# Optimization experiments

Hardware: AMD Instinct MI355X
Metric: run time of the kernel (lower is better)

Reference implementation:

```python
import jax, jax.numpy as jnp
import numpy as np

EMBED_DIM = 1024
NUM_HEADS = 16
HEAD_DIM = EMBED_DIM // NUM_HEADS
LN_EPS = 1e-5


def setup_inputs() -> dict:
    key = jax.random.key(0)
    ks = jax.random.split(key, 5)
    N, L, C = 32, 577, EMBED_DIM
    x = jax.random.normal(ks[0], (N, L, C), dtype=jnp.float32)
    ln1_g = jnp.ones((C,), dtype=jnp.float32)
    ln1_b = jnp.zeros((C,), dtype=jnp.float32)
    w_in = jax.random.normal(ks[1], (3 * C, C), dtype=jnp.float32) * (C ** -0.5)
    b_in = jax.random.normal(ks[2], (3 * C,), dtype=jnp.float32) * 0.02
    w_out = jax.random.normal(ks[3], (C, C), dtype=jnp.float32) * (C ** -0.5)
    b_out = jax.random.normal(ks[4], (C,), dtype=jnp.float32) * 0.02
    return {"x": x, "ln1_g": ln1_g, "ln1_b": ln1_b, "w_in": w_in,
            "b_in": b_in, "w_out": w_out, "b_out": b_out}


def _layernorm(x, g, b):
    mu = jnp.mean(x, axis=-1, keepdims=True)
    var = jnp.mean(jnp.square(x - mu), axis=-1, keepdims=True)
    return (x - mu) * jax.lax.rsqrt(var + LN_EPS) * g + b


def reference(x, ln1_g, ln1_b, w_in, b_in, w_out, b_out):
    # ClearCLIP last block, attn_variant='qq', keep_residual=False, keep_ffn=False.
    N, L, C = x.shape
    H, D = NUM_HEADS, HEAD_DIM
    z = _layernorm(x, ln1_g, ln1_b)
    qkv = z @ w_in.T + b_in                      # (N, L, 3C)
    q, k, v = jnp.split(qkv, 3, axis=-1)
    k = q                                        # 'qq' self-self variant
    def heads(t):
        return t.reshape(N, L, H, D).transpose(0, 2, 1, 3)  # (N, H, L, D)
    q, k, v = heads(q), heads(k), heads(v)
    scale = 1.0 / np.sqrt(D).astype(np.float32)
    scores = jnp.einsum('nhld,nhsd->nhls', q, k) * scale    # (N, H, L, L)
    attn = jax.nn.softmax(scores, axis=-1)
    out = jnp.einsum('nhls,nhsd->nhld', attn, v)            # (N, H, L, D)
    out = out.transpose(0, 2, 1, 3).reshape(N, L, C)
    return out @ w_out.T + b_out                 # ls_1 = Identity, no residual/FFN
```

## Files before the change

### kernel.cpp

```cpp
#include <hip/hip_runtime.h>
#include <stdint.h>

typedef short bf16x8 __attribute__((ext_vector_type(8)));
typedef float f32x4 __attribute__((ext_vector_type(4)));
typedef unsigned int uint4v __attribute__((ext_vector_type(4)));
typedef unsigned short ushort4v __attribute__((ext_vector_type(4)));
typedef float float4v __attribute__((ext_vector_type(4)));

#define MROWS 18464
#define SEQ   577
#define CDIM  1024
#define SPAD  640
#define W1ELEMS (2048*1024)
#define W2ELEMS (1024*1024)
#define SQC 0.42466089f

__device__ __forceinline__ unsigned short f2bf(float f) {
  unsigned int u = __float_as_uint(f);
  u += 0x7fffu + ((u >> 16) & 1u);
  return (unsigned short)(u >> 16);
}

__device__ __forceinline__ void load_lds16(const void* g, void* lds) {
  __builtin_amdgcn_global_load_lds(
      (const __attribute__((address_space(1))) unsigned int*)(uint64_t)(uintptr_t)g,
      (__attribute__((address_space(3))) unsigned int*)(unsigned int)(uintptr_t)lds,
      16, 0, 0);
}

__global__ __launch_bounds__(256) void ln_kernel(const float* __restrict__ x,
                                                 const float* __restrict__ g,
                                                 const float* __restrict__ b,
                                                 unsigned short* __restrict__ z) {
  const int row = blockIdx.x;
  const int t = threadIdx.x;
  const float4v v = *(const float4v*)(x + (size_t)row * CDIM + t * 4);
  float s  = v[0] + v[1] + v[2] + v[3];
  float ss = v[0]*v[0] + v[1]*v[1] + v[2]*v[2] + v[3]*v[3];
  #pragma unroll
  for (int off = 1; off < 64; off <<= 1) { s += __shfl_xor(s, off); ss += __shfl_xor(ss, off); }
  __shared__ float rs[4], rss[4];
  const int w = t >> 6, l = t & 63;
  if (l == 0) { rs[w] = s; rss[w] = ss; }
  __syncthreads();
  s = rs[0] + rs[1] + rs[2] + rs[3];
  ss = rss[0] + rss[1] + rss[2] + rss[3];
  const float mu = s * (1.0f / CDIM);
  const float var = ss * (1.0f / CDIM) - mu * mu;
  const float rstd = rsqrtf(var + 1e-5f);
  const float4v gv = *(const float4v*)(g + t * 4);
  const float4v bv = *(const float4v*)(b + t * 4);
  ushort4v o;
  #pragma unroll
  for (int j = 0; j < 4; ++j) o[j] = f2bf((v[j] - mu) * rstd * gv[j] + bv[j]);
  *(ushort4v*)(z + (size_t)row * CDIM + t * 4) = o;
}

__global__ __launch_bounds__(256) void conv_kernel(const float* __restrict__ w_in,
                                                   const float* __restrict__ w_out,
                                                   unsigned short* __restrict__ wqv,
                                                   unsigned short* __restrict__ wo,
                                                   unsigned short* __restrict__ vt) {
  const int idx = blockIdx.x * 256 + threadIdx.x;
  const int e = idx * 4;
  if (e < W1ELEMS) {
    const int row = e >> 10;
    const int srow = row < 1024 ? row : row + 1024;
    const float4v v = *(const float4v*)(w_in + (size_t)srow * 1024 + (e & 1023));
    ushort4v o;
    #pragma unroll
    for (int j = 0; j < 4; ++j) o[j] = f2bf(v[j]);
    *(ushort4v*)(wqv + e) = o;
  } else if (e < W1ELEMS + W2ELEMS) {
    const int e2 = e - W1ELEMS;
    const float4v v = *(const float4v*)(w_out + e2);
    ushort4v o;
    #pragma unroll
    for (int j = 0; j < 4; ++j) o[j] = f2bf(v[j]);
    *(ushort4v*)(wo + e2) = o;
  } else {
    const int pidx = idx - (W1ELEMS + W2ELEMS) / 4;
    const int ic = pidx >> 3, part = pidx & 7;
    *(uint4v*)(vt + (size_t)ic * SPAD + 576 + part * 8) = (uint4v)0u;
  }
}

template<int MODE>
__global__ __launch_bounds__(512, 2) void gemm256(const unsigned short* __restrict__ A,
                                                  const unsigned short* __restrict__ B,
                                                  const float* __restrict__ bias,
                                                  void* __restrict__ outp,
                                                  unsigned short* __restrict__ vtout) {
  __shared__ char smem[131072];
  const int t = threadIdx.x;
  const int w = t >> 6, l = t & 63;
  int p, c;
  if constexpr (MODE == 0) {
    const int L = (blockIdx.x & 7) * 73 + (blockIdx.x >> 3);
    p = L >> 3; c = L & 7;
  } else {
    const int xcd = blockIdx.x & 7, j = blockIdx.x >> 3;
    const int L = (xcd < 4 ? xcd * 37 : 148 + (xcd - 4) * 36) + j;
    p = L >> 2; c = L & 3;
  }
  const int m0 = p * 256;
  const int n0 = c * 256;
  const int wm = w >> 2, wn = w & 3;
  const int g4 = (l >> 4) * 4;
  const int fr = l & 15;
  const int fb = (l >> 4) * 16;
  const int sw = (l & 7) << 4;

  f32x4 acc[8][4];
  #pragma unroll
  for (int i = 0; i < 8; ++i)
    #pragma unroll
    for (int j = 0; j < 4; ++j) acc[i][j] = (f32x4)0.0f;

  const int srow = l >> 3;
  const int scol = ((((l & 7) * 16) ^ ((srow & 7) << 4)) >> 1);
  const unsigned short* Ap[4];
  const unsigned short* Bp[4];
  #pragma unroll
  for (int c2 = 0; c2 < 4; ++c2) {
    int arow = m0 + w * 32 + c2 * 8 + srow;
    if (arow > MROWS - 1) arow = MROWS - 1;
    Ap[c2] = A + (size_t)arow * 1024 + scol;
    Bp[c2] = B + (size_t)(n0 + w * 32 + c2 * 8 + srow) * 1024 + scol;
  }

  #define STG(kt, buf)                                                     \
    {                                                                      \
      char* const d_ = smem + (buf) * 65536 + w * 4096;                    \
      const int k0_ = (kt) * 64;                                           \
      _Pragma("unroll")                                                    \
      for (int c2 = 0; c2 < 4; ++c2) {                                     \
        load_lds16(Ap[c2] + k0_, d_ + c2 * 1024);                          \
        load_lds16(Bp[c2] + k0_, d_ + 32768 + c2 * 1024);                  \
      }                                                                    \
    }

  STG(0, 0)
  __syncthreads();

  for (int kb = 0; kb < 16; ++kb) {
    const int b = kb & 1;
    if (kb < 15) STG(kb + 1, b ^ 1)
    const char* Ab = smem + b * 65536;
    const char* Bb = Ab + 32768;
    #pragma unroll
    for (int kk = 0; kk < 2; ++kk) {
      bf16x8 af[8], bfr[4];
      #pragma unroll
      for (int i = 0; i < 8; ++i)
        af[i] = *(const bf16x8*)(Ab + (wm * 128 + i * 16 + fr) * 128 + ((kk * 64 + fb) ^ sw));
      #pragma unroll
      for (int j = 0; j < 4; ++j)
        bfr[j] = *(const bf16x8*)(Bb + (wn * 64 + j * 16 + fr) * 128 + ((kk * 64 + fb) ^ sw));
      #pragma unroll
      for (int i = 0; i < 8; ++i)
        #pragma unroll
        for (int j = 0; j < 4; ++j)
          acc[i][j] = __builtin_amdgcn_mfma_f32_16x16x32_bf16(af[i], bfr[j], acc[i][j], 0, 0, 0);
    }
    __syncthreads();
  }
  #undef STG

  if constexpr (MODE == 0) {
    unsigned short* sm = (unsigned short*)smem;
    const bool isq = (n0 < 1024);
    const float* bb = isq ? (bias + n0) : (bias + 1024 + n0);
    const float scl = isq ? SQC : 1.0f;
    float bcol[4];
    #pragma unroll
    for (int j = 0; j < 4; ++j) bcol[j] = bb[wn * 64 + j * 16 + fr];
    for (int pass = 0; pass < 2; ++pass) {
      if (wm == pass) {
        #pragma unroll
        for (int i = 0; i < 8; ++i)
          #pragma unroll
          for (int j = 0; j < 4; ++j)
            #pragma unroll
            for (int r = 0; r < 4; ++r)
              sm[(i * 16 + g4 + r) * 264 + wn * 64 + j * 16 + fr] =
                  f2bf((acc[i][j][r] + bcol[j]) * scl);
      }
      __syncthreads();
      if (isq) {
        unsigned short* o = (unsigned short*)outp;
        #pragma unroll
        for (int it = 0; it < 8; ++it) {
          const int cid = it * 512 + t;
          const int row = cid >> 5, ch = cid & 31;
          const int grow = m0 + pass * 128 + row;
          if (grow < MROWS)
            *(uint4v*)(o + (size_t)grow * 1024 + n0 + ch * 8) =
                *(const uint4v*)(sm + row * 264 + ch * 8);
        }
      } else {
        const int rowloc = t & 127, chb = t >> 7;
        const int token = m0 + pass * 128 + rowloc;
        if (token < MROWS) {
          const unsigned int nimg = (unsigned int)token / 577u;
          const int s = token - (int)(nimg * 577u);
          unsigned short* op =
              vtout + ((size_t)nimg * 1024 + (n0 - 1024) + chb * 64) * SPAD + s;
          const unsigned short* sp = sm + rowloc * 264 + chb * 64;
          #pragma unroll 8
          for (int it = 0; it < 64; ++it)
            op[(size_t)it * SPAD] = sp[it];
        }
      }
      __syncthreads();
    }
  } else {
    float* smf = (float*)smem;
    float bcol[4];
    #pragma unroll
    for (int j = 0; j < 4; ++j) bcol[j] = bias[n0 + wn * 64 + j * 16 + fr];
    float* o = (float*)outp;
    for (int q4 = 0; q4 < 4; ++q4) {
      if (wm == (q4 >> 1)) {
        const int i0 = (q4 & 1) * 4;
        #pragma unroll
        for (int i2 = 0; i2 < 4; ++i2)
          #pragma unroll
          for (int j = 0; j < 4; ++j)
            #pragma unroll
            for (int r = 0; r < 4; ++r)
              smf[(i2 * 16 + g4 + r) * 260 + wn * 64 + j * 16 + fr] =
                  acc[i0 + i2][j][r] + bcol[j];
      }
      __syncthreads();
      #pragma unroll
      for (int it = 0; it < 8; ++it) {
        const int cid = it * 512 + t;
        const int row = cid >> 6, ch = cid & 63;
        const int grow = m0 + q4 * 64 + row;
        if (grow < MROWS)
          *(float4v*)(o + (size_t)grow * 1024 + n0 + ch * 4) =
              *(const float4v*)(smf + row * 260 + ch * 4);
      }
      __syncthreads();
    }
  }
}

__global__ __launch_bounds__(256) void attn_kernel(const unsigned short* __restrict__ qbuf,
                                                   const unsigned short* __restrict__ vt,
                                                   unsigned short* __restrict__ out) {
  __shared__ char smem[32768];
  const int t = threadIdx.x, w = t >> 6, l = t & 63;
  const int g = l >> 4, fr = l & 15;
  const int bid = blockIdx.x;
  const int xcd = bid & 7, idx = bid >> 3;
  const int nhl = idx / 5;
  const int qb = idx - nhl * 5;
  const int nh = xcd * 64 + nhl;
  const int n = nh >> 4, h = nh & 15;
  const size_t rowbase = (size_t)n * SEQ;
  const int sw = (l & 7) << 4;

  bf16x8 bq[2][2];
  #pragma unroll
  for (int half = 0; half < 2; ++half) {
    const unsigned short* qp =
        qbuf + (rowbase + qb * 128 + half * 64 + w * 16 + fr) * 1024 + h * 64 + g * 8;
    bq[half][0] = *(const bf16x8*)qp;
    bq[half][1] = *(const bf16x8*)(qp + 32);
  }

  const int srow = l >> 3;
  const int scolE = ((((l & 7) * 16) ^ ((srow & 7) << 4)) >> 1);
  const unsigned short* ksrc = qbuf + (rowbase + w * 16 + srow) * 1024 + h * 64 + scolE;
  const unsigned short* vsrc = vt + ((size_t)nh * 64 + w * 16 + srow) * SPAD + scolE;

  f32x4 acc[2][4];
  #pragma unroll
  for (int half = 0; half < 2; ++half)
    #pragma unroll
    for (int cf = 0; cf < 4; ++cf) acc[half][cf] = (f32x4)0.0f;
  float l_run[2] = {0.0f, 0.0f};

  {
    char* kdst = smem + (w * 16) * 128;
    char* vdst = smem + 8192 + (w * 16) * 128;
    load_lds16(ksrc, kdst);
    load_lds16(ksrc + (size_t)8 * 1024, kdst + 1024);
    load_lds16(vsrc, vdst);
    load_lds16(vsrc + 8 * SPAD, vdst + 1024);
  }
  __syncthreads();

  for (int kb = 0; kb < 10; ++kb) {
    const int b = kb & 1;
    const char* kbuf = smem + b * 16384;
    const char* vbuf = kbuf + 8192;

    if (kb < 9) {
      char* kdst = smem + (b ^ 1) * 16384 + (w * 16) * 128;
      char* vdst = kdst + 8192;
      load_lds16(ksrc + (size_t)((kb + 1) * 64) * 1024, kdst);
      load_lds16(ksrc + (size_t)((kb + 1) * 64 + 8) * 1024, kdst + 1024);
      load_lds16(vsrc + (kb + 1) * 64, vdst);
      load_lds16(vsrc + 8 * SPAD + (kb + 1) * 64, vdst + 1024);
    }

    f32x4 s4[2][4];
    #pragma unroll
    for (int half = 0; half < 2; ++half)
      #pragma unroll
      for (int cf = 0; cf < 4; ++cf) s4[half][cf] = (f32x4)0.0f;
    #pragma unroll
    for (int kk = 0; kk < 2; ++kk)
      #pragma unroll
      for (int cf = 0; cf < 4; ++cf) {
        const bf16x8 af = *(const bf16x8*)(kbuf + (cf * 16 + fr) * 128 + ((kk * 64 + g * 16) ^ sw));
        s4[0][cf] = __builtin_amdgcn_mfma_f32_16x16x32_bf16(af, bq[0][kk], s4[0][cf], 0, 0, 0);
        s4[1][cf] = __builtin_amdgcn_mfma_f32_16x16x32_bf16(af, bq[1][kk], s4[1][cf], 0, 0, 0);
      }

    if (kb == 9) {
      #pragma unroll
      for (int half = 0; half < 2; ++half) {
        #pragma unroll
        for (int cf = 0; cf < 4; ++cf)
          #pragma unroll
          for (int r = 0; r < 4; ++r)
            if (cf != 0 || r != 0) s4[half][cf][r] = -__builtin_inff();
        s4[half][0][0] = (g == 0) ? s4[half][0][0] : -__builtin_inff();
      }
    }

    bf16x8 ap[2][2];
    #pragma unroll
    for (int half = 0; half < 2; ++half) {
      float sum = 0.0f;
      #pragma unroll
      for (int cf = 0; cf < 4; ++cf)
        #pragma unroll
        for (int r = 0; r < 4; ++r) {
          const float p2 = __builtin_amdgcn_exp2f(s4[half][cf][r]);
          s4[half][cf][r] = p2;
          sum += p2;
        }
      sum += __shfl_xor(sum, 16);
      sum += __shfl_xor(sum, 32);
      l_run[half] += sum;

      unsigned int pka[4], pkb[4];
      #pragma unroll
      for (int cf = 0; cf < 4; ++cf) {
        asm("v_cvt_pk_bf16_f32 %0, %1, %2" : "=v"(pka[cf]) : "v"(s4[half][cf][0]), "v"(s4[half][cf][1]));
        asm("v_cvt_pk_bf16_f32 %0, %1, %2" : "=v"(pkb[cf]) : "v"(s4[half][cf][2]), "v"(s4[half][cf][3]));
      }
      #pragma unroll
      for (int kk = 0; kk < 2; ++kk) {
        unsigned int a0 = pka[2 * kk], b0 = pka[2 * kk + 1];
        unsigned int a1 = pkb[2 * kk], b1 = pkb[2 * kk + 1];
        asm("v_permlane32_swap_b32 %0, %1" : "+v"(a0), "+v"(b0));
        asm("v_permlane16_swap_b32 %0, %1" : "+v"(a0), "+v"(b0));
        asm("v_permlane32_swap_b32 %0, %1" : "+v"(a1), "+v"(b1));
        asm("v_permlane16_swap_b32 %0, %1" : "+v"(a1), "+v"(b1));
        union { unsigned int i[4]; bf16x8 v; } u;
        u.i[0] = a0; u.i[1] = a1; u.i[2] = b0; u.i[3] = b1;
        ap[half][kk] = u.v;
      }
    }

    #pragma unroll
    for (int kk = 0; kk < 2; ++kk)
      #pragma unroll
      for (int cf = 0; cf < 4; ++cf) {
        const bf16x8 bv = *(const bf16x8*)(vbuf + (cf * 16 + fr) * 128 + ((kk * 64 + g * 16) ^ sw));
        acc[0][cf] = __builtin_amdgcn_mfma_f32_16x16x32_bf16(ap[0][kk], bv, acc[0][cf], 0, 0, 0);
        acc[1][cf] = __builtin_amdgcn_mfma_f32_16x16x32_bf16(ap[1][kk], bv, acc[1][cf], 0, 0, 0);
      }

    __syncthreads();
  }

  #pragma unroll
  for (int half = 0; half < 2; ++half) {
    const float rcp = 1.0f / l_run[half];
    #pragma unroll
    for (int r = 0; r < 4; ++r) {
      const float rr = __shfl(rcp, g * 4 + r);
      const int qg = qb * 128 + half * 64 + w * 16 + g * 4 + r;
      if (qg < SEQ) {
        #pragma unroll
        for (int cf = 0; cf < 4; ++cf)
          out[(rowbase + qg) * 1024 + h * 64 + cf * 16 + fr] = f2bf(acc[half][cf][r] * rr);
      }
    }
  }
}

extern "C" void kernel_launch(void* const* d_in, const int* in_sizes, int n_in,
                              void* d_out, int out_size, void* d_ws, size_t ws_size,
                              hipStream_t stream) {
  const float* x     = (const float*)d_in[0];
  const float* ln_g  = (const float*)d_in[1];
  const float* ln_b  = (const float*)d_in[2];
  const float* w_in  = (const float*)d_in[3];
  const float* b_in  = (const float*)d_in[4];
  const float* w_out = (const float*)d_in[5];
  const float* b_out = (const float*)d_in[6];

  unsigned short* z    = (unsigned short*)d_ws;
  unsigned short* qbuf = z + (size_t)MROWS * 1024;
  unsigned short* vt   = qbuf + (size_t)MROWS * 1024;
  unsigned short* wqv  = vt + (size_t)512 * 64 * SPAD;
  unsigned short* wo   = wqv + (size_t)2048 * 1024;

  ln_kernel<<<MROWS, 256, 0, stream>>>(x, ln_g, ln_b, z);
  conv_kernel<<<4096, 256, 0, stream>>>(w_in, w_out, wqv, wo, vt);
  gemm256<0><<<584, 512, 0, stream>>>(z, wqv, b_in, qbuf, vt);
  attn_kernel<<<2560, 256, 0, stream>>>(qbuf, vt, z);
  gemm256<1><<<292, 512, 0, stream>>>(z, wo, b_out, d_out, nullptr);
}
```

Before: 250.7 us.

## Interleave GEMM main loop into fine-grained load/MFMA phases with setprio

Rewrites the 256x256 bf16 GEMM main loop into an eight-phase, hand-scheduled pipeline. Each phase reads half-tiles from LDS, issues partial global-to-LDS stages for the next k-tiles, and runs a 4x4 MFMA cluster. Explicit vmcnt waits and raw s_barrier calls replace the per-iteration __syncthreads, and s_setprio raises priority around MFMA bursts. The goal is to overlap global loads, LDS reads and matrix math more tightly and to cut register pressure from holding 8 A fragments. In exchange it adds many more barriers and relies on fragile manual wait counts and buffer hazards.

```diff
diff --git a/kernel.cpp b/kernel.cpp
--- a/kernel.cpp
+++ b/kernel.cpp
@@ -103,8 +103,7 @@
     const int L = (xcd < 4 ? xcd * 37 : 148 + (xcd - 4) * 36) + j;
     p = L >> 2; c = L & 3;
   }
-  const int m0 = p * 256;
-  const int n0 = c * 256;
+  const int m0 = p * 256, n0 = c * 256;
   const int wm = w >> 2, wn = w & 3;
   const int g4 = (l >> 4) * 4;
   const int fr = l & 15;
@@ -119,53 +118,90 @@
 
   const int srow = l >> 3;
   const int scol = ((((l & 7) * 16) ^ ((srow & 7) << 4)) >> 1);
-  const unsigned short* Ap[4];
-  const unsigned short* Bp[4];
-  #pragma unroll
-  for (int c2 = 0; c2 < 4; ++c2) {
-    int arow = m0 + w * 32 + c2 * 8 + srow;
-    if (arow > MROWS - 1) arow = MROWS - 1;
-    Ap[c2] = A + (size_t)arow * 1024 + scol;
-    Bp[c2] = B + (size_t)(n0 + w * 32 + c2 * 8 + srow) * 1024 + scol;
-  }
-
-  #define STG(kt, buf)                                                     \
-    {                                                                      \
-      char* const d_ = smem + (buf) * 65536 + w * 4096;                    \
-      const int k0_ = (kt) * 64;                                           \
-      _Pragma("unroll")                                                    \
-      for (int c2 = 0; c2 < 4; ++c2) {                                     \
-        load_lds16(Ap[c2] + k0_, d_ + c2 * 1024);                          \
-        load_lds16(Bp[c2] + k0_, d_ + 32768 + c2 * 1024);                  \
-      }                                                                    \
-    }
-
-  STG(0, 0)
+  const int alr = (w < 4) ? w * 16 : 128 + (w - 4) * 16;
+
+  int r0 = m0 + alr + srow;       if (r0 > MROWS - 1) r0 = MROWS - 1;
+  int r1 = m0 + alr + 8 + srow;   if (r1 > MROWS - 1) r1 = MROWS - 1;
+  int r2 = m0 + alr + 64 + srow;  if (r2 > MROWS - 1) r2 = MROWS - 1;
+  int r3 = m0 + alr + 72 + srow;  if (r3 > MROWS - 1) r3 = MROWS - 1;
+  const unsigned short* pAL0 = A + (size_t)r0 * 1024 + scol;
+  const unsigned short* pAL1 = A + (size_t)r1 * 1024 + scol;
+  const unsigned short* pAH0 = A + (size_t)r2 * 1024 + scol;
+  const unsigned short* pAH1 = A + (size_t)r3 * 1024 + scol;
+  const unsigned short* pB00 = B + (size_t)(n0 + w * 16 + srow) * 1024 + scol;
+  const unsigned short* pB01 = pB00 + 8 * 1024;
+  const unsigned short* pB10 = pB00 + 128 * 1024;
+  const unsigned short* pB11 = pB00 + 136 * 1024;
+
+  char* const dAL0 = smem + alr * 128;
+  char* const dAH0 = dAL0 + 64 * 128;
+  char* const dAL1 = dAL0 + 65536;
+  char* const dAH1 = dAH0 + 65536;
+  char* const dB0s0 = smem + 32768 + (w * 16) * 128;
+  char* const dB1s0 = dB0s0 + 128 * 128;
+  char* const dB0s1 = dB0s0 + 65536;
+  char* const dB1s1 = dB1s0 + 65536;
+
+  #define STGH(pp0, pp1, dd, kt) { load_lds16((pp0) + (kt) * 64, (dd)); load_lds16((pp1) + (kt) * 64, (dd) + 1024); }
+  #define VMC(n) { asm volatile("s_waitcnt vmcnt(" #n ")" ::: "memory"); __builtin_amdgcn_sched_barrier(0); }
+  #define BAR __builtin_amdgcn_s_barrier();
+  #define RD_A(dst, so, ho, kk) \
+    _Pragma("unroll") for (int i2 = 0; i2 < 4; ++i2) \
+      dst[i2] = *(const bf16x8*)(smem + (so) + (wm * 128 + (ho) + i2 * 16 + fr) * 128 + (((kk) * 64 + fb) ^ sw));
+  #define RD_B(dst, so, kk) \
+    _Pragma("unroll") for (int j2 = 0; j2 < 4; ++j2) \
+      dst[j2] = *(const bf16x8*)(smem + (so) + 32768 + (wn * 64 + j2 * 16 + fr) * 128 + (((kk) * 64 + fb) ^ sw));
+  #define MMA(I0, AF, BF) \
+    __builtin_amdgcn_s_setprio(1); \
+    _Pragma("unroll") for (int i2 = 0; i2 < 4; ++i2) \
+      _Pragma("unroll") for (int j2 = 0; j2 < 4; ++j2) \
+        acc[(I0) + i2][j2] = __builtin_amdgcn_mfma_f32_16x16x32_bf16(AF[i2], BF[j2], acc[(I0) + i2][j2], 0, 0, 0); \
+    __builtin_amdgcn_s_setprio(0);
+
+  STGH(pB00, pB01, dB0s0, 0) STGH(pB10, pB11, dB1s0, 0)
+  STGH(pAL0, pAL1, dAL0, 0)  STGH(pAH0, pAH1, dAH0, 0)
+  STGH(pB00, pB01, dB0s1, 1) STGH(pB10, pB11, dB1s1, 1)
+  STGH(pAL0, pAL1, dAL1, 1)  STGH(pAH0, pAH1, dAH1, 1)
+  VMC(4)
+  BAR
+
+  bf16x8 afL[4], afH[4], bf0[4], bf1[4];
+  for (int i = 0; i < 8; ++i) {
+    const int kA = 2 * i + 2;
+    const int kB = 2 * i + 1;
+    const int kC = 2 * i + 3;
+    RD_B(bf0, 0, 0) RD_A(afL, 0, 0, 0)
+    if (i > 0) STGH(pB10, pB11, dB1s1, kB)
+    BAR MMA(0, afL, bf0) VMC(4) BAR
+    RD_A(afH, 0, 64, 0)
+    if (i > 0) STGH(pAL0, pAL1, dAL1, kB)
+    BAR MMA(4, afH, bf0) BAR
+    RD_B(bf1, 0, 1) RD_A(afL, 0, 0, 1)
+    if (i > 0) STGH(pAH0, pAH1, dAH1, kB)
+    BAR MMA(0, afL, bf1) BAR
+    RD_A(afH, 0, 64, 1)
+    if (i < 7) STGH(pB00, pB01, dB0s0, kA)
+    BAR MMA(4, afH, bf1) VMC(2) BAR
+    RD_B(bf0, 65536, 0) RD_A(afL, 65536, 0, 0)
+    if (i < 7) STGH(pB10, pB11, dB1s0, kA)
+    BAR MMA(0, afL, bf0) VMC(4) BAR
+    RD_A(afH, 65536, 64, 0)
+    if (i < 7) STGH(pAL0, pAL1, dAL0, kA)
+    BAR MMA(4, afH, bf0) BAR
+    RD_B(bf1, 65536, 1) RD_A(afL, 65536, 0, 1)
+    if (i < 7) STGH(pAH0, pAH1, dAH0, kA)
+    BAR MMA(0, afL, bf1) BAR
+    RD_A(afH, 65536, 64, 1)
+    if (i < 7) STGH(pB00, pB01, dB0s1, kC)
+    BAR MMA(4, afH, bf1) VMC(4) BAR
+  }
+  #undef STGH
+  #undef VMC
+  #undef BAR
+  #undef RD_A
+  #undef RD_B
+  #undef MMA
   __syncthreads();
-
-  for (int kb = 0; kb < 16; ++kb) {
-    const int b = kb & 1;
-    if (kb < 15) STG(kb + 1, b ^ 1)
-    const char* Ab = smem + b * 65536;
-    const char* Bb = Ab + 32768;
-    #pragma unroll
-    for (int kk = 0; kk < 2; ++kk) {
-      bf16x8 af[8], bfr[4];
-      #pragma unroll
-      for (int i = 0; i < 8; ++i)
-        af[i] = *(const bf16x8*)(Ab + (wm * 128 + i * 16 + fr) * 128 + ((kk * 64 + fb) ^ sw));
-      #pragma unroll
-      for (int j = 0; j < 4; ++j)
-        bfr[j] = *(const bf16x8*)(Bb + (wn * 64 + j * 16 + fr) * 128 + ((kk * 64 + fb) ^ sw));
-      #pragma unroll
-      for (int i = 0; i < 8; ++i)
-        #pragma unroll
-        for (int j = 0; j < 4; ++j)
-          acc[i][j] = __builtin_amdgcn_mfma_f32_16x16x32_bf16(af[i], bfr[j], acc[i][j], 0, 0, 0);
-    }
-    __syncthreads();
-  }
-  #undef STG
 
   if constexpr (MODE == 0) {
     unsigned short* sm = (unsigned short*)smem;
```

After: 261.5 us. 1.04x slower.
